# Performance work log

Measured on AMD Instinct MI355X. Metric: run time of the kernel, lower is better.

The kernel has to match this reference:

```python
import jax, jax.numpy as jnp
import numpy as np


def _squash(t):
    # squash along axis=2 (the atoms axis of [B, D, A, 1, 1])
    norm = jnp.linalg.norm(t, axis=2, keepdims=True)
    n2 = norm * norm
    return t / norm * (n2 / (1.0 + n2))


def setup_inputs() -> dict:
    key = jax.random.key(0)
    k1, k2 = jax.random.split(key)
    B, I, Ain, D, A = 32, 2048, 16, 32, 16
    x = jax.random.normal(k1, (B, I, Ain, 1, 1), jnp.float32)
    weights = 0.1 * jax.random.normal(k2, (I, Ain, D * A, 1, 1), jnp.float32)
    bias = jnp.full((D, A, 1, 1), 0.1, jnp.float32)  # nn.init.constant_(0.1)
    return {"x": x, "weights": weights, "bias": bias, "num_routing": 3}


def reference(x, weights, bias, num_routing):
    B, I, Ain = x.shape[:3]
    D, A = bias.shape[:2]
    # Vote computation (standard voting): sum over input_atoms.
    # Torch does expand+mul+sum; einsum is the same math without the 4.8GB intermediate.
    votes = jnp.einsum('bia,iao->bio', x[:, :, :, 0, 0],
                       weights[:, :, :, 0, 0]).reshape(B, I, D, A, 1, 1)
    votes_sg = jax.lax.stop_gradient(votes)  # votes_trans_stopped in torch
    logits = jnp.zeros((B, I, D, 1, 1), x.dtype)
    activation = None
    for i in range(num_routing):
        route = jax.nn.softmax(logits, axis=2)  # [B, I, D, 1, 1], softmax over D
        v = votes if i == num_routing - 1 else votes_sg
        # route broadcast over atoms axis; sum over input capsules I
        preact = jnp.sum(route[:, :, :, None] * v, axis=1) + bias  # [B, D, A, 1, 1]
        activation = _squash(preact)
        if i < num_routing - 1:
            # agreement update uses non-stopped votes (as in torch)
            logits = logits + jnp.sum(votes * activation[:, None], axis=3)  # [B, I, D, 1, 1]
    return activation
```

## Files before the change

### kernel.cpp

```cpp
#include <hip/hip_runtime.h>


#define B_  32
#define I_  2048
#define K_  16
#define O_  512
#define KO_ (K_ * O_)
#define NG_ 256
#define IC_ 8

typedef const __attribute__((address_space(1))) uint32_t* gp_t;
typedef __attribute__((address_space(3))) uint32_t* lp_t;

__device__ __forceinline__
void stage_tile(const float* __restrict__ g, float* dst, int wave, int lane)
{
    #pragma unroll
    for (int q = 0; q < 8; ++q) {
        const int c = wave * 8 + q;
        __builtin_amdgcn_global_load_lds(
            (gp_t)(g + c * 256 + lane * 4),
            (lp_t)(dst + c * 256), 16, 0, 0);
    }
}

template<bool ROUTED>
__global__ __launch_bounds__(256)
void sweep_kernel(const float* __restrict__ x, const float* __restrict__ W,
                  const float* __restrict__ act, float* __restrict__ partial)
{
    const int tid  = threadIdx.x;
    const int lane = tid & 63;
    const int wave = tid >> 6;
    const int ig   = blockIdx.x >> 1;
    const int bh   = blockIdx.x & 1;
    const int wv    = __builtin_amdgcn_readfirstlane(wave);
    const int bbase = bh * 16 + wv * 4;
    const int ob1  = lane * 4;
    const int ob2  = 256 + lane * 4;
    const int ibase = ig * IC_;

    __shared__ float sW[2 * KO_];

    stage_tile(W + (size_t)ibase * KO_, sW, wave, lane);

    float facc[4][8];
    #pragma unroll
    for (int bb = 0; bb < 4; ++bb)
        #pragma unroll
        for (int j = 0; j < 8; ++j) facc[bb][j] = 0.f;

    float as[4][8];
    if (ROUTED) {
        #pragma unroll
        for (int bb = 0; bb < 4; ++bb) {
            const float4 f0 = *(const float4*)(act + (bbase + bb) * O_ + ob1);
            const float4 f1 = *(const float4*)(act + (bbase + bb) * O_ + ob2);
            as[bb][0]=f0.x; as[bb][1]=f0.y; as[bb][2]=f0.z; as[bb][3]=f0.w;
            as[bb][4]=f1.x; as[bb][5]=f1.y; as[bb][6]=f1.z; as[bb][7]=f1.w;
        }
    }

    for (int r = 0; r < IC_; ++r) {
        const int i = ibase + r;
        __syncthreads();
        if (r + 1 < IC_)
            stage_tile(W + (size_t)(i + 1) * KO_, sW + ((r + 1) & 1) * KO_,
                       wave, lane);

        float xs[4][16];
        #pragma unroll
        for (int bb = 0; bb < 4; ++bb) {
            const float4* xp =
                (const float4*)(x + ((size_t)(bbase + bb) * I_ + i) * K_);
            #pragma unroll
            for (int q = 0; q < 4; ++q) {
                float4 v = xp[q];
                xs[bb][4*q+0]=v.x; xs[bb][4*q+1]=v.y;
                xs[bb][4*q+2]=v.z; xs[bb][4*q+3]=v.w;
            }
        }

        const float* buf = sW + (r & 1) * KO_;
        float V[4][8];
        #pragma unroll
        for (int bb = 0; bb < 4; ++bb)
            #pragma unroll
            for (int j = 0; j < 8; ++j) V[bb][j] = 0.f;
        #pragma unroll
        for (int k = 0; k < K_; ++k) {
            const float4 w0 = *(const float4*)&buf[k * O_ + ob1];
            const float4 w1 = *(const float4*)&buf[k * O_ + ob2];
            #pragma unroll
            for (int bb = 0; bb < 4; ++bb) {
                const float xb = xs[bb][k];
                V[bb][0] = fmaf(xb, w0.x, V[bb][0]);
                V[bb][1] = fmaf(xb, w0.y, V[bb][1]);
                V[bb][2] = fmaf(xb, w0.z, V[bb][2]);
                V[bb][3] = fmaf(xb, w0.w, V[bb][3]);
                V[bb][4] = fmaf(xb, w1.x, V[bb][4]);
                V[bb][5] = fmaf(xb, w1.y, V[bb][5]);
                V[bb][6] = fmaf(xb, w1.z, V[bb][6]);
                V[bb][7] = fmaf(xb, w1.w, V[bb][7]);
            }
        }

        #pragma unroll
        for (int bb = 0; bb < 4; ++bb) {
            if (!ROUTED) {
                #pragma unroll
                for (int j = 0; j < 8; ++j) facc[bb][j] += V[bb][j];
            } else {
                float p1 = 0.f, p2 = 0.f;
                #pragma unroll
                for (int j = 0; j < 4; ++j) {
                    p1 = fmaf(V[bb][j],     as[bb][j],     p1);
                    p2 = fmaf(V[bb][j + 4], as[bb][j + 4], p2);
                }
                p1 += __shfl_xor(p1, 1);  p1 += __shfl_xor(p1, 2);
                p2 += __shfl_xor(p2, 1);  p2 += __shfl_xor(p2, 2);
                const float e1 = __expf(p1);
                const float e2 = __expf(p2);
                float s = e1 + e2;
                s += __shfl_xor(s, 4);
                s += __shfl_xor(s, 8);
                s += __shfl_xor(s, 16);
                s += __shfl_xor(s, 32);
                const float inv = __builtin_amdgcn_rcpf(s);
                const float r1 = e1 * inv, r2 = e2 * inv;
                #pragma unroll
                for (int j = 0; j < 4; ++j) {
                    facc[bb][j]     = fmaf(r1, V[bb][j],     facc[bb][j]);
                    facc[bb][j + 4] = fmaf(r2, V[bb][j + 4], facc[bb][j + 4]);
                }
            }
        }
    }

    #pragma unroll
    for (int bb = 0; bb < 4; ++bb) {
        const int b = bbase + bb;
        *(float4*)&partial[((size_t)ig * B_ + b) * O_ + ob1] =
            make_float4(facc[bb][0], facc[bb][1], facc[bb][2], facc[bb][3]);
        *(float4*)&partial[((size_t)ig * B_ + b) * O_ + ob2] =
            make_float4(facc[bb][4], facc[bb][5], facc[bb][6], facc[bb][7]);
    }
}

__global__ __launch_bounds__(256)
void reduce_squash(const float* __restrict__ partial, const float* __restrict__ bias,
                   float scale, const float* __restrict__ addbase,
                   float* __restrict__ dst)
{
    const int t     = threadIdx.x;
    const int gbase = blockIdx.x * 32;
    const int q     = t & 7;
    const int sl    = t >> 3;
    const float4* src = (const float4*)partial + (gbase >> 2) + q;

    float4 acc = make_float4(0.f, 0.f, 0.f, 0.f);
    #pragma unroll
    for (int r = 0; r < 8; ++r) {
        float4 v = src[(size_t)(sl * 8 + r) * (B_ * O_ / 4)];
        acc.x += v.x; acc.y += v.y; acc.z += v.z; acc.w += v.w;
    }
    __shared__ float4 red[256];
    red[t] = acc;
    __syncthreads();
    if (t < 32) {
        float v = 0.f;
        #pragma unroll
        for (int s = 0; s < 32; ++s)
            v += ((const float*)&red[s * 8 + (t >> 2)])[t & 3];
        const float p = fmaf(v, scale, bias[(gbase + t) & (O_ - 1)]);
        float nn = p * p;
        nn += __shfl_xor(nn, 1);
        nn += __shfl_xor(nn, 2);
        nn += __shfl_xor(nn, 4);
        nn += __shfl_xor(nn, 8);
        float o = p * sqrtf(nn) / (1.f + nn);
        if (addbase) o += addbase[gbase + t];
        dst[gbase + t] = o;
    }
}

extern "C" void kernel_launch(void* const* d_in, const int* in_sizes, int n_in,
                              void* d_out, int out_size, void* d_ws, size_t ws_size,
                              hipStream_t stream) {
    const float* x    = (const float*)d_in[0];
    const float* W    = (const float*)d_in[1];
    const float* bias = (const float*)d_in[2];
    float* out = (float*)d_out;

    float* partial = (float*)d_ws;
    float* act0    = partial + (size_t)NG_ * B_ * O_;
    float* asum    = act0 + B_ * O_;

    sweep_kernel<false><<<NG_ * 2, 256, 0, stream>>>(x, W, nullptr, partial);
    reduce_squash<<<512, 256, 0, stream>>>(partial, bias, 1.f / 32.f, nullptr, act0);
    sweep_kernel<true><<<NG_ * 2, 256, 0, stream>>>(x, W, act0, partial);
    reduce_squash<<<512, 256, 0, stream>>>(partial, bias, 1.f, act0, asum);
    sweep_kernel<true><<<NG_ * 2, 256, 0, stream>>>(x, W, asum, partial);
    reduce_squash<<<512, 256, 0, stream>>>(partial, bias, 1.f, nullptr, out);
}
```

Measured before the change: 195.4 us.

## Load weights directly into registers with software prefetch instead of LDS staging

Drops the LDS double-buffered weight staging (global_load_lds plus __syncthreads per input capsule). Each wave now loads its weight float4s straight from global memory into a two-slot register buffer, prefetching the next 4-k chunk while computing the current one. This removes the block barriers and LDS traffic. In exchange, the 4 waves of a block each fetch the same weights separately, relying on cache, and register pressure rises.

```diff
diff --git a/kernel.cpp b/kernel.cpp
--- a/kernel.cpp
+++ b/kernel.cpp
@@ -8,21 +8,6 @@
 #define KO_ (K_ * O_)
 #define NG_ 256
 #define IC_ 8
-
-typedef const __attribute__((address_space(1))) uint32_t* gp_t;
-typedef __attribute__((address_space(3))) uint32_t* lp_t;
-
-__device__ __forceinline__
-void stage_tile(const float* __restrict__ g, float* dst, int wave, int lane)
-{
-    #pragma unroll
-    for (int q = 0; q < 8; ++q) {
-        const int c = wave * 8 + q;
-        __builtin_amdgcn_global_load_lds(
-            (gp_t)(g + c * 256 + lane * 4),
-            (lp_t)(dst + c * 256), 16, 0, 0);
-    }
-}
 
 template<bool ROUTED>
 __global__ __launch_bounds__(256)
@@ -40,10 +25,6 @@
     const int ob2  = 256 + lane * 4;
     const int ibase = ig * IC_;
 
-    __shared__ float sW[2 * KO_];
-
-    stage_tile(W + (size_t)ibase * KO_, sW, wave, lane);
-
     float facc[4][8];
     #pragma unroll
     for (int bb = 0; bb < 4; ++bb)
@@ -61,12 +42,18 @@
         }
     }
 
-    for (int r = 0; r < IC_; ++r) {
-        const int i = ibase + r;
-        __syncthreads();
-        if (r + 1 < IC_)
-            stage_tile(W + (size_t)(i + 1) * KO_, sW + ((r + 1) & 1) * KO_,
-                       wave, lane);
+    const float4* wp4 = (const float4*)W + (size_t)ibase * (KO_ / 4) + lane;
+
+    float4 wreg[2][8];
+    #pragma unroll
+    for (int u = 0; u < 4; ++u) {
+        wreg[0][2*u]   = wp4[u * 128];
+        wreg[0][2*u+1] = wp4[u * 128 + 64];
+    }
+
+    for (int ii = 0; ii < IC_; ++ii) {
+        const int i = ibase + ii;
+        const float4* wcur  = wp4 + (size_t)ii * 2048;
 
         float xs[4][16];
         #pragma unroll
@@ -81,27 +68,45 @@
             }
         }
 
-        const float* buf = sW + (r & 1) * KO_;
         float V[4][8];
         #pragma unroll
         for (int bb = 0; bb < 4; ++bb)
             #pragma unroll
             for (int j = 0; j < 8; ++j) V[bb][j] = 0.f;
-        #pragma unroll
-        for (int k = 0; k < K_; ++k) {
-            const float4 w0 = *(const float4*)&buf[k * O_ + ob1];
-            const float4 w1 = *(const float4*)&buf[k * O_ + ob2];
+
+        #pragma unroll
+        for (int c = 0; c < 4; ++c) {
+            const int cur = c & 1, nxt = cur ^ 1;
+            if (c < 3) {
+                #pragma unroll
+                for (int u = 0; u < 4; ++u) {
+                    wreg[nxt][2*u]   = wcur[(c+1) * 4 * 128 + u * 128];
+                    wreg[nxt][2*u+1] = wcur[(c+1) * 4 * 128 + u * 128 + 64];
+                }
+            } else if (ii + 1 < IC_) {
+                #pragma unroll
+                for (int u = 0; u < 4; ++u) {
+                    wreg[nxt][2*u]   = wcur[2048 + u * 128];
+                    wreg[nxt][2*u+1] = wcur[2048 + u * 128 + 64];
+                }
+            }
             #pragma unroll
-            for (int bb = 0; bb < 4; ++bb) {
-                const float xb = xs[bb][k];
-                V[bb][0] = fmaf(xb, w0.x, V[bb][0]);
-                V[bb][1] = fmaf(xb, w0.y, V[bb][1]);
-                V[bb][2] = fmaf(xb, w0.z, V[bb][2]);
-                V[bb][3] = fmaf(xb, w0.w, V[bb][3]);
-                V[bb][4] = fmaf(xb, w1.x, V[bb][4]);
-                V[bb][5] = fmaf(xb, w1.y, V[bb][5]);
-                V[bb][6] = fmaf(xb, w1.z, V[bb][6]);
-                V[bb][7] = fmaf(xb, w1.w, V[bb][7]);
+            for (int u = 0; u < 4; ++u) {
+                const float4 w0 = wreg[cur][2*u];
+                const float4 w1 = wreg[cur][2*u+1];
+                const int k = c * 4 + u;
+                #pragma unroll
+                for (int bb = 0; bb < 4; ++bb) {
+                    const float xb = xs[bb][k];
+                    V[bb][0] = fmaf(xb, w0.x, V[bb][0]);
+                    V[bb][1] = fmaf(xb, w0.y, V[bb][1]);
+                    V[bb][2] = fmaf(xb, w0.z, V[bb][2]);
+                    V[bb][3] = fmaf(xb, w0.w, V[bb][3]);
+                    V[bb][4] = fmaf(xb, w1.x, V[bb][4]);
+                    V[bb][5] = fmaf(xb, w1.y, V[bb][5]);
+                    V[bb][6] = fmaf(xb, w1.z, V[bb][6]);
+                    V[bb][7] = fmaf(xb, w1.w, V[bb][7]);
+                }
             }
         }
 
```

Result: no change. 194.6 us (-0.4%).
